# Kernel tuning notes

Hardware: AMD Instinct MI355X
Metric: run time of the kernel (lower is better)

The kernel has to match this reference:

```python
import jax, jax.numpy as jnp
import numpy as np

NODE_NUM = 20000
NUM_CENTROIDS = 64
EMBED_SIZE = 128
EPS = 1e-5
POINT_SCALE = 0.1 / np.sqrt(EMBED_SIZE)  # keep Poincare-ball norms << 1


def setup_inputs() -> dict:
    key = jax.random.key(0)
    k1, k2 = jax.random.split(key)
    node_repr = jax.random.normal(k1, (NODE_NUM, EMBED_SIZE), dtype=jnp.float32) * POINT_SCALE
    centroid_weight = jax.random.normal(k2, (NUM_CENTROIDS, EMBED_SIZE), dtype=jnp.float32) * POINT_SCALE
    mask = jnp.ones((NODE_NUM, 1), dtype=jnp.float32)
    return {"node_repr": node_repr, "mask": mask, "centroid_weight": centroid_weight}


def _poincare_pairwise_dist(u, v):
    # u: [N, E], v: [C, E] -> [N, C]
    # d(u,v) = arccosh(1 + 2*||u-v||^2 / ((1-||u||^2)(1-||v||^2)))
    su = jnp.sum(u * u, axis=-1)                      # [N]
    sv = jnp.sum(v * v, axis=-1)                      # [C]
    dot = jnp.einsum('ne,ce->nc', u, v)               # [N, C]
    sqdist = su[:, None] + sv[None, :] - 2.0 * dot    # ||u-v||^2, [N, C]
    sqdist = jnp.maximum(sqdist, 0.0)
    denom = jnp.maximum((1.0 - su)[:, None] * (1.0 - sv)[None, :], EPS)
    arg = jnp.maximum(1.0 + 2.0 * sqdist / denom, 1.0 + EPS)
    return jnp.arccosh(arg)


def reference(node_repr, mask, centroid_weight):
    node_num = node_repr.shape[0]
    num_centroids = centroid_weight.shape[0]
    # fused pairwise manifold distance, no [N*C, E] materialization
    dist = _poincare_pairwise_dist(node_repr, centroid_weight)      # [N, C]
    node_centroid_dist = dist[None, :, :] * mask[None, :, :]        # [1, N, C] (mask broadcasts [N,1])
    graph_centroid_dist = jnp.sum(node_centroid_dist, axis=1) / jnp.sum(mask)  # [1, C]
    return (graph_centroid_dist, node_centroid_dist)
```

## Files before the change

### kernel.cpp

```cpp
#include <hip/hip_runtime.h>
#include <hip/hip_bf16.h>
#include <math.h>

#define EMBED  128
#define NUM_C  64
#define EPS    1e-5f
#define NPB    32

typedef __attribute__((ext_vector_type(8))) short bf16x8;
typedef __attribute__((ext_vector_type(4))) float f32x4;

__device__ __forceinline__ bf16x8 pack8(float4 x, float4 y) {
    __hip_bfloat162 p0 = __float22bfloat162_rn(float2{x.x, x.y});
    __hip_bfloat162 p1 = __float22bfloat162_rn(float2{x.z, x.w});
    __hip_bfloat162 p2 = __float22bfloat162_rn(float2{y.x, y.y});
    __hip_bfloat162 p3 = __float22bfloat162_rn(float2{y.z, y.w});
    union { __hip_bfloat162 h[4]; bf16x8 v; } u;
    u.h[0] = p0; u.h[1] = p1; u.h[2] = p2; u.h[3] = p3;
    return u.v;
}

__global__ __launch_bounds__(256) void cd_main(
    const float* __restrict__ node_repr,
    const float* __restrict__ mask,
    const float* __restrict__ cent,
    float* __restrict__ out,
    float* __restrict__ wcol,
    float* __restrict__ wmsk,
    int N, int nb, int atomicMode)
{
    const int tid  = threadIdx.x;
    const int lane = tid & 63;
    const int wv   = tid >> 6;
    const int quad = lane >> 4;
    const int lm   = lane & 15;
    const int cw   = wv * 16;
    const int node0 = blockIdx.x * NPB;

    const float* ap = cent + (long)(cw + lm) * EMBED + quad * 8;
    float svp = 0.f;
    bf16x8 aa[4];
    #pragma unroll
    for (int ks = 0; ks < 4; ++ks) {
        float4 a0 = *(const float4*)(ap + ks * 32);
        float4 a1 = *(const float4*)(ap + ks * 32 + 4);
        svp = fmaf(a0.x,a0.x, fmaf(a0.y,a0.y, fmaf(a0.z,a0.z, fmaf(a0.w,a0.w, svp))));
        svp = fmaf(a1.x,a1.x, fmaf(a1.y,a1.y, fmaf(a1.z,a1.z, fmaf(a1.w,a1.w, svp))));
        aa[ks] = pack8(a0, a1);
    }
    svp += __shfl_xor(svp, 16); svp += __shfl_xor(svp, 32);
    float svr[4], sv1r[4];
    #pragma unroll
    for (int r = 0; r < 4; ++r) {
        svr[r]  = __shfl(svp, quad * 4 + r);
        sv1r[r] = 1.f - svr[r];
    }

    const int n0 = node0 + lm;
    const int n1 = node0 + 16 + lm;
    const int c0 = (n0 < N) ? n0 : N - 1;
    const int c1 = (n1 < N) ? n1 : N - 1;
    const float* p0 = node_repr + (long)c0 * EMBED + quad * 8;
    const float* p1 = node_repr + (long)c1 * EMBED + quad * 8;
    float su0 = 0.f, su1 = 0.f;
    bf16x8 b0[4], b1[4];
    #pragma unroll
    for (int ks = 0; ks < 4; ++ks) {
        float4 x0 = *(const float4*)(p0 + ks * 32);
        float4 x1 = *(const float4*)(p0 + ks * 32 + 4);
        float4 y0 = *(const float4*)(p1 + ks * 32);
        float4 y1 = *(const float4*)(p1 + ks * 32 + 4);
        su0 = fmaf(x0.x,x0.x, fmaf(x0.y,x0.y, fmaf(x0.z,x0.z, fmaf(x0.w,x0.w, su0))));
        su0 = fmaf(x1.x,x1.x, fmaf(x1.y,x1.y, fmaf(x1.z,x1.z, fmaf(x1.w,x1.w, su0))));
        su1 = fmaf(y0.x,y0.x, fmaf(y0.y,y0.y, fmaf(y0.z,y0.z, fmaf(y0.w,y0.w, su1))));
        su1 = fmaf(y1.x,y1.x, fmaf(y1.y,y1.y, fmaf(y1.z,y1.z, fmaf(y1.w,y1.w, su1))));
        b0[ks] = pack8(x0, x1);
        b1[ks] = pack8(y0, y1);
    }
    su0 += __shfl_xor(su0, 16); su0 += __shfl_xor(su0, 32);
    su1 += __shfl_xor(su1, 16); su1 += __shfl_xor(su1, 32);
    const float mk0 = (n0 < N) ? mask[c0] : 0.f;
    const float mk1 = (n1 < N) ? mask[c1] : 0.f;

    f32x4 acc0 = {0.f,0.f,0.f,0.f}, acc1 = {0.f,0.f,0.f,0.f};
    #pragma unroll
    for (int ks = 0; ks < 4; ++ks) {
        acc0 = __builtin_amdgcn_mfma_f32_16x16x32_bf16(aa[ks], b0[ks], acc0, 0, 0, 0);
        acc1 = __builtin_amdgcn_mfma_f32_16x16x32_bf16(aa[ks], b1[ks], acc1, 0, 0, 0);
    }

    const float o0 = 1.f - su0, o1 = 1.f - su1;
    float v0a[4], v1a[4], g[4];
    #pragma unroll
    for (int r = 0; r < 4; ++r) {
        {
            float sq = fmaxf(su0 + svr[r] - 2.f * acc0[r], 0.f);
            float dn = fmaxf(o0 * sv1r[r], EPS);
            float tt = fmaxf(2.f * sq * __builtin_amdgcn_rcpf(dn), EPS);
            v0a[r] = __logf(1.f + tt + sqrtf(tt * (tt + 2.f))) * mk0;
        }
        {
            float sq = fmaxf(su1 + svr[r] - 2.f * acc1[r], 0.f);
            float dn = fmaxf(o1 * sv1r[r], EPS);
            float tt = fmaxf(2.f * sq * __builtin_amdgcn_rcpf(dn), EPS);
            v1a[r] = __logf(1.f + tt + sqrtf(tt * (tt + 2.f))) * mk1;
        }
        g[r] = v0a[r] + v1a[r];
    }
    if (n0 < N) {
        float4 V0 = {v0a[0], v0a[1], v0a[2], v0a[3]};
        *(float4*)(out + NUM_C + (long)n0 * NUM_C + cw + quad * 4) = V0;
    }
    if (n1 < N) {
        float4 V1 = {v1a[0], v1a[1], v1a[2], v1a[3]};
        *(float4*)(out + NUM_C + (long)n1 * NUM_C + cw + quad * 4) = V1;
    }

    #pragma unroll
    for (int r = 0; r < 4; ++r) {
        g[r] += __shfl_xor(g[r], 1);
        g[r] += __shfl_xor(g[r], 2);
        g[r] += __shfl_xor(g[r], 4);
        g[r] += __shfl_xor(g[r], 8);
    }
    if (lm == 0) {
        if (atomicMode) {
            #pragma unroll
            for (int r = 0; r < 4; ++r) atomicAdd(&wcol[cw + quad * 4 + r], g[r]);
        } else {
            #pragma unroll
            for (int r = 0; r < 4; ++r)
                wcol[(long)(cw + quad * 4 + r) * nb + blockIdx.x] = g[r];
        }
    }

    if (wv == 0) {
        float ms = mk0 + mk1;
        ms += __shfl_xor(ms, 1); ms += __shfl_xor(ms, 2);
        ms += __shfl_xor(ms, 4); ms += __shfl_xor(ms, 8);
        if (lane == 0) {
            if (atomicMode) atomicAdd(&wmsk[0], ms);
            else            wmsk[blockIdx.x] = ms;
        }
    }
}

__global__ __launch_bounds__(256) void cd_fin1(
    const float* __restrict__ wcol, const float* __restrict__ wmsk,
    float* __restrict__ out, int nb)
{
    __shared__ float rs[4], rm[4];
    const int c   = blockIdx.x;
    const int tid = threadIdx.x;

    float s = 0.f, m = 0.f;
    for (int b = tid; b < nb; b += 256) {
        s += wcol[(long)c * nb + b];
        m += wmsk[b];
    }
    #pragma unroll
    for (int k = 32; k; k >>= 1) { s += __shfl_xor(s, k, 64); m += __shfl_xor(m, k, 64); }
    if ((tid & 63) == 0) { rs[tid >> 6] = s; rm[tid >> 6] = m; }
    __syncthreads();
    if (tid == 0)
        out[c] = (rs[0] + rs[1] + rs[2] + rs[3]) / (rm[0] + rm[1] + rm[2] + rm[3]);
}

__global__ void cd_zero(float* acc) { if (threadIdx.x < NUM_C + 1) acc[threadIdx.x] = 0.f; }
__global__ void cd_fin_atomic(const float* __restrict__ acc, float* __restrict__ out) {
    int c = threadIdx.x;
    if (c < NUM_C) out[c] = acc[c] / acc[NUM_C];
}

extern "C" void kernel_launch(void* const* d_in, const int* in_sizes, int n_in,
                              void* d_out, int out_size, void* d_ws, size_t ws_size,
                              hipStream_t stream) {
    const float* node_repr = (const float*)d_in[0];
    const float* mask      = (const float*)d_in[1];
    const float* cent      = (const float*)d_in[2];
    float* out = (float*)d_out;

    const int N  = in_sizes[0] / EMBED;
    const int nb = (N + NPB - 1) / NPB;
    const size_t needed = ((size_t)NUM_C * nb + nb) * sizeof(float);

    if (ws_size >= needed) {
        float* wcol = (float*)d_ws;
        float* wmsk = wcol + (size_t)NUM_C * nb;
        cd_main<<<nb, 256, 0, stream>>>(node_repr, mask, cent, out, wcol, wmsk, N, nb, 0);
        cd_fin1<<<NUM_C, 256, 0, stream>>>(wcol, wmsk, out, nb);
    } else {
        float* acc = (float*)d_ws;
        cd_zero<<<1, 128, 0, stream>>>(acc);
        cd_main<<<nb, 256, 0, stream>>>(node_repr, mask, cent, out, acc, acc + NUM_C, N, nb, 1);
        cd_fin_atomic<<<1, 64, 0, stream>>>(acc, out);
    }
}
```

Baseline: 74.30 us.

## Stage node tile in LDS once per block instead of per-wave global loads

Each block now loads its 32 node rows from global memory once into shared memory, computing row norms and mask values during staging. The four waves then read their MFMA operands from LDS instead of each wave reloading the same node rows from global memory. This cuts redundant global reads fourfold, at the cost of a __syncthreads barrier and about 17KB of LDS per block, which may reduce occupancy.

```diff
diff --git a/kernel.cpp b/kernel.cpp
--- a/kernel.cpp
+++ b/kernel.cpp
@@ -6,6 +6,7 @@
 #define NUM_C  64
 #define EPS    1e-5f
 #define NPB    32
+#define LDSROW 132
 
 typedef __attribute__((ext_vector_type(8))) short bf16x8;
 typedef __attribute__((ext_vector_type(4))) float f32x4;
@@ -29,6 +30,10 @@
     float* __restrict__ wmsk,
     int N, int nb, int atomicMode)
 {
+    __shared__ float sa[NPB * LDSROW];
+    __shared__ float s_su[NPB];
+    __shared__ float s_ms[NPB];
+
     const int tid  = threadIdx.x;
     const int lane = tid & 63;
     const int wv   = tid >> 6;
@@ -37,6 +42,33 @@
     const int cw   = wv * 16;
     const int node0 = blockIdx.x * NPB;
 
+    const int srow = tid >> 3;
+    const int scol = (tid & 7) * 16;
+    {
+        int row = node0 + srow;
+        int rc  = row < N ? row : N - 1;
+        const float* p = node_repr + (long)rc * EMBED + scol;
+        float4 r0 = *(const float4*)(p);
+        float4 r1 = *(const float4*)(p + 4);
+        float4 r2 = *(const float4*)(p + 8);
+        float4 r3 = *(const float4*)(p + 12);
+        float mrow = (row < N) ? mask[rc] : 0.f;
+
+        float* dst = &sa[srow * LDSROW + scol];
+        *(float4*)(dst)      = r0;
+        *(float4*)(dst + 4)  = r1;
+        *(float4*)(dst + 8)  = r2;
+        *(float4*)(dst + 12) = r3;
+
+        float pp = 0.f;
+        pp = fmaf(r0.x,r0.x, fmaf(r0.y,r0.y, fmaf(r0.z,r0.z, fmaf(r0.w,r0.w, pp))));
+        pp = fmaf(r1.x,r1.x, fmaf(r1.y,r1.y, fmaf(r1.z,r1.z, fmaf(r1.w,r1.w, pp))));
+        pp = fmaf(r2.x,r2.x, fmaf(r2.y,r2.y, fmaf(r2.z,r2.z, fmaf(r2.w,r2.w, pp))));
+        pp = fmaf(r3.x,r3.x, fmaf(r3.y,r3.y, fmaf(r3.z,r3.z, fmaf(r3.w,r3.w, pp))));
+        pp += __shfl_xor(pp, 1); pp += __shfl_xor(pp, 2); pp += __shfl_xor(pp, 4);
+        if ((tid & 7) == 0) { s_su[srow] = pp; s_ms[srow] = mrow; }
+    }
+
     const float* ap = cent + (long)(cw + lm) * EMBED + quad * 8;
     float svp = 0.f;
     bf16x8 aa[4];
@@ -56,40 +88,25 @@
         sv1r[r] = 1.f - svr[r];
     }
 
-    const int n0 = node0 + lm;
-    const int n1 = node0 + 16 + lm;
-    const int c0 = (n0 < N) ? n0 : N - 1;
-    const int c1 = (n1 < N) ? n1 : N - 1;
-    const float* p0 = node_repr + (long)c0 * EMBED + quad * 8;
-    const float* p1 = node_repr + (long)c1 * EMBED + quad * 8;
-    float su0 = 0.f, su1 = 0.f;
-    bf16x8 b0[4], b1[4];
+    __syncthreads();
+
+    f32x4 acc0 = {0.f,0.f,0.f,0.f}, acc1 = {0.f,0.f,0.f,0.f};
     #pragma unroll
     for (int ks = 0; ks < 4; ++ks) {
-        float4 x0 = *(const float4*)(p0 + ks * 32);
-        float4 x1 = *(const float4*)(p0 + ks * 32 + 4);
-        float4 y0 = *(const float4*)(p1 + ks * 32);
-        float4 y1 = *(const float4*)(p1 + ks * 32 + 4);
-        su0 = fmaf(x0.x,x0.x, fmaf(x0.y,x0.y, fmaf(x0.z,x0.z, fmaf(x0.w,x0.w, su0))));
-        su0 = fmaf(x1.x,x1.x, fmaf(x1.y,x1.y, fmaf(x1.z,x1.z, fmaf(x1.w,x1.w, su0))));
-        su1 = fmaf(y0.x,y0.x, fmaf(y0.y,y0.y, fmaf(y0.z,y0.z, fmaf(y0.w,y0.w, su1))));
-        su1 = fmaf(y1.x,y1.x, fmaf(y1.y,y1.y, fmaf(y1.z,y1.z, fmaf(y1.w,y1.w, su1))));
-        b0[ks] = pack8(x0, x1);
-        b1[ks] = pack8(y0, y1);
-    }
-    su0 += __shfl_xor(su0, 16); su0 += __shfl_xor(su0, 32);
-    su1 += __shfl_xor(su1, 16); su1 += __shfl_xor(su1, 32);
-    const float mk0 = (n0 < N) ? mask[c0] : 0.f;
-    const float mk1 = (n1 < N) ? mask[c1] : 0.f;
-
-    f32x4 acc0 = {0.f,0.f,0.f,0.f}, acc1 = {0.f,0.f,0.f,0.f};
-    #pragma unroll
-    for (int ks = 0; ks < 4; ++ks) {
-        acc0 = __builtin_amdgcn_mfma_f32_16x16x32_bf16(aa[ks], b0[ks], acc0, 0, 0, 0);
-        acc1 = __builtin_amdgcn_mfma_f32_16x16x32_bf16(aa[ks], b1[ks], acc1, 0, 0, 0);
-    }
-
-    const float o0 = 1.f - su0, o1 = 1.f - su1;
+        const int base = quad * 8 + ks * 32;
+        float4 b00 = *(const float4*)&sa[lm * LDSROW + base];
+        float4 b01 = *(const float4*)&sa[lm * LDSROW + base + 4];
+        float4 b10 = *(const float4*)&sa[(16 + lm) * LDSROW + base];
+        float4 b11 = *(const float4*)&sa[(16 + lm) * LDSROW + base + 4];
+        acc0 = __builtin_amdgcn_mfma_f32_16x16x32_bf16(aa[ks], pack8(b00, b01), acc0, 0, 0, 0);
+        acc1 = __builtin_amdgcn_mfma_f32_16x16x32_bf16(aa[ks], pack8(b10, b11), acc1, 0, 0, 0);
+    }
+
+    const float su0 = s_su[lm],      su1 = s_su[16 + lm];
+    const float mk0 = s_ms[lm],      mk1 = s_ms[16 + lm];
+    const float o0  = 1.f - su0,     o1  = 1.f - su1;
+    const int   n0  = node0 + lm,    n1  = node0 + 16 + lm;
+
     float v0a[4], v1a[4], g[4];
     #pragma unroll
     for (int r = 0; r < 4; ++r) {
@@ -135,9 +152,9 @@
     }
 
     if (wv == 0) {
-        float ms = mk0 + mk1;
-        ms += __shfl_xor(ms, 1); ms += __shfl_xor(ms, 2);
-        ms += __shfl_xor(ms, 4); ms += __shfl_xor(ms, 8);
+        float ms = (lane < NPB) ? s_ms[lane] : 0.f;
+        #pragma unroll
+        for (int k = 32; k; k >>= 1) ms += __shfl_xor(ms, k, 64);
         if (lane == 0) {
             if (atomicMode) atomicAdd(&wmsk[0], ms);
             else            wmsk[blockIdx.x] = ms;
```

Result: faster. 71.43 us (-3.9%).
